# Optimization experiments

Hardware: AMD Instinct MI355X
Metric: run time of the kernel (lower is better)

The kernel has to match this reference:

```python
import jax, jax.numpy as jnp
import numpy as np

H = 256        # hidden_size
MAX_LEN = 200  # position table has MAX_LEN+1 rows
B = 4096       # number of sessions


def setup_inputs() -> dict:
    rng = np.random.RandomState(0)
    # ragged session lengths in [10, 100)
    seq_len = rng.randint(10, 100, size=B).astype(np.int64)
    T = int(seq_len.sum())
    # reverse positions: len-1, ..., 1, 0 per session (as the torch code uses)
    reverse_pos = np.concatenate([np.arange(l - 1, -1, -1) for l in seq_len]).astype(np.int64)

    key = jax.random.key(0)
    ks = jax.random.split(key, 8)
    def lin(k, fin, fout):
        # torch Linear init ~ U(-1/sqrt(fin), 1/sqrt(fin)); store as [fin, fout]
        lim = 1.0 / np.sqrt(fin)
        kw, kb = jax.random.split(k)
        W = jax.random.uniform(kw, (fin, fout), jnp.float32, -lim, lim)
        b = jax.random.uniform(kb, (fout,), jnp.float32, -lim, lim)
        return W, b

    hidden = jax.random.normal(ks[0], (T, H), jnp.float32)
    pos_table = jax.random.normal(ks[1], (MAX_LEN + 1, H), jnp.float32)
    W_pos, b_pos = lin(ks[2], 2 * H, H)   # W_pos_inter
    W1, b1 = lin(ks[3], H, H)             # W_1_inter
    W2, b2 = lin(ks[4], H, H)             # W_2_inter
    qw, qb = lin(ks[5], H, 1)             # q_inter

    return {
        "hidden": hidden,
        "pos_table": pos_table,
        "W_pos": W_pos, "b_pos": b_pos,
        "W1": W1, "b1": b1,
        "W2": W2, "b2": b2,
        "qw": qw, "qb": qb,
        "seq_len": jnp.asarray(seq_len),
        "reverse_pos": jnp.asarray(reverse_pos),
    }


def reference(hidden, pos_table, W_pos, b_pos, W1, b1, W2, b2, qw, qb, seq_len, reverse_pos):
    T = hidden.shape[0]
    nb = seq_len.shape[0]
    # segment id per token (sessions are contiguous)
    seg = jnp.repeat(jnp.arange(nb), seq_len, total_repeat_length=T)  # [T]
    # per-session mean, gathered back per token (v_mean_repeat_concat)
    sess_mean = jax.ops.segment_sum(hidden, seg, num_segments=nb)
    sess_mean = sess_mean / seq_len[:, None].astype(hidden.dtype)
    v_mean = sess_mean[seg]                                           # [T, H]
    # position-augmented hidden: tanh(W_pos_inter([hidden; pos_emb]))
    pos_emb = pos_table[reverse_pos]                                  # [T, H]
    pos_hidden = jnp.tanh(jnp.concatenate([hidden, pos_emb], -1) @ W_pos + b_pos)
    # alpha = q_inter(sigmoid(W_1_inter(v_mean) + W_2_inter(pos_hidden)))
    gate = jax.nn.sigmoid(v_mean @ W1 + b1 + pos_hidden @ W2 + b2)
    alpha = gate @ qw + qb                                            # [T, 1]
    # per-session weighted sum of hidden
    h_s = jax.ops.segment_sum(alpha * hidden, seg, num_segments=nb)   # [B, H]
    return h_s
```

## Files before the change

kernel.cpp:

```cpp
#include <hip/hip_runtime.h>
#include <hip/hip_bf16.h>
#include <stdint.h>

#define HD 256
#define BM 128
#define APAD 8
#define ASTRIDE (HD + APAD)

typedef __bf16 bf16x8 __attribute__((ext_vector_type(8)));
typedef float f32x4 __attribute__((ext_vector_type(4)));
typedef unsigned short ushort8v __attribute__((ext_vector_type(8)));
typedef unsigned short us4 __attribute__((ext_vector_type(4)));

__device__ __forceinline__ unsigned short f2bf(float f) {
    unsigned int x = __float_as_uint(f);
    unsigned int r = (x + 0x7FFFu + ((x >> 16) & 1u)) >> 16;
    return (unsigned short)r;
}

__global__ void scan_kernel(const int* __restrict__ seq_len, int* __restrict__ offsets, int B) {
    __shared__ int sums[256];
    int tid = threadIdx.x;
    int per = (B + 255) / 256;
    int b0 = tid * per;
    int local[32];
    int tot = 0;
    for (int i = 0; i < per && i < 32; ++i) {
        int b = b0 + i;
        int v = (b < B) ? seq_len[b] : 0;
        local[i] = tot;
        tot += v;
    }
    sums[tid] = tot;
    __syncthreads();
    for (int off = 1; off < 256; off <<= 1) {
        int v = (tid >= off) ? sums[tid - off] : 0;
        __syncthreads();
        sums[tid] += v;
        __syncthreads();
    }
    int start = sums[tid] - tot;
    for (int i = 0; i < per && i < 32; ++i) {
        int b = b0 + i;
        if (b < B) offsets[b] = start + local[i];
    }
    if (tid == 255) offsets[B] = sums[255];
}

__global__ void mean_kernel(const float* __restrict__ hidden, const int* __restrict__ offsets,
                            unsigned short* __restrict__ mean_bf, unsigned short* __restrict__ hb,
                            int* __restrict__ seg) {
    int b = blockIdx.x;
    int s = offsets[b], e = offsets[b + 1];
    int tid = threadIdx.x;
    for (int t = s + tid; t < e; t += 256) seg[t] = b;
    int g = tid >> 6, c = tid & 63;
    float4 acc = {0.f, 0.f, 0.f, 0.f};
    for (int t = s + g; t < e; t += 4) {
        const float4 v = *reinterpret_cast<const float4*>(hidden + (size_t)t * HD + c * 4);
        acc.x += v.x; acc.y += v.y; acc.z += v.z; acc.w += v.w;
        if (hb) {
            us4 pk;
            pk[0] = f2bf(v.x); pk[1] = f2bf(v.y); pk[2] = f2bf(v.z); pk[3] = f2bf(v.w);
            *reinterpret_cast<us4*>(hb + (size_t)t * HD + c * 4) = pk;
        }
    }
    __shared__ float4 part[4][64];
    part[g][c] = acc;
    __syncthreads();
    if (g == 0) {
        float4 a0 = part[0][c], a1 = part[1][c], a2 = part[2][c], a3 = part[3][c];
        float inv = 1.0f / (float)(e - s);
        us4 pk;
        pk[0] = f2bf((a0.x + a1.x + a2.x + a3.x) * inv);
        pk[1] = f2bf((a0.y + a1.y + a2.y + a3.y) * inv);
        pk[2] = f2bf((a0.z + a1.z + a2.z + a3.z) * inv);
        pk[3] = f2bf((a0.w + a1.w + a2.w + a3.w) * inv);
        *reinterpret_cast<us4*>(mean_bf + (size_t)b * HD + c * 4) = pk;
    }
}

__global__ void transpose_kernel(const float* __restrict__ Wp, const float* __restrict__ W1,
                                 const float* __restrict__ W2,
                                 unsigned short* __restrict__ WphT, unsigned short* __restrict__ WpbT,
                                 unsigned short* __restrict__ W1T, unsigned short* __restrict__ W2T) {
    int n = blockIdx.x;
    int k = threadIdx.x;
    WphT[n * HD + k] = f2bf(Wp[k * HD + n]);
    WpbT[n * HD + k] = f2bf(Wp[(HD + k) * HD + n]);
    W1T[n * HD + k]  = f2bf(W1[k * HD + n]);
    W2T[n * HD + k]  = f2bf(W2[k * HD + n]);
}

__global__ __launch_bounds__(256) void small_gemm_kernel(
    const unsigned short* __restrict__ mean_bf, int Mu, int nbu,
    const float* __restrict__ pos_table, int Mp,
    const unsigned short* __restrict__ W1T, const unsigned short* __restrict__ WpbT,
    const float* __restrict__ b1, const float* __restrict__ b2, const float* __restrict__ bp,
    float* __restrict__ u, float* __restrict__ P2) {
    __shared__ __align__(16) unsigned short As[16][ASTRIDE];
    int tid = threadIdx.x;
    bool isU = (int)blockIdx.x < nbu;
    int m0 = isU ? blockIdx.x * 16 : (blockIdx.x - nbu) * 16;
    int M  = isU ? Mu : Mp;
    const unsigned short* BT = isU ? W1T : WpbT;
    float* out = isU ? u : P2;

    {
        int row = tid >> 4;
        int colg = (tid & 15) * 16;
        int m = m0 + row;
        if (isU) {
            ushort8v v0 = {0,0,0,0,0,0,0,0}, v1 = {0,0,0,0,0,0,0,0};
            if (m < M) {
                v0 = *reinterpret_cast<const ushort8v*>(mean_bf + (size_t)m * HD + colg);
                v1 = *reinterpret_cast<const ushort8v*>(mean_bf + (size_t)m * HD + colg + 8);
            }
            *reinterpret_cast<ushort8v*>(&As[row][colg])     = v0;
            *reinterpret_cast<ushort8v*>(&As[row][colg + 8]) = v1;
        } else {
            float4 f[4] = {{0,0,0,0},{0,0,0,0},{0,0,0,0},{0,0,0,0}};
            if (m < M) {
                const float4* p = reinterpret_cast<const float4*>(pos_table + (size_t)m * HD + colg);
                f[0] = p[0]; f[1] = p[1]; f[2] = p[2]; f[3] = p[3];
            }
            ushort8v v0, v1;
            v0[0]=f2bf(f[0].x); v0[1]=f2bf(f[0].y); v0[2]=f2bf(f[0].z); v0[3]=f2bf(f[0].w);
            v0[4]=f2bf(f[1].x); v0[5]=f2bf(f[1].y); v0[6]=f2bf(f[1].z); v0[7]=f2bf(f[1].w);
            v1[0]=f2bf(f[2].x); v1[1]=f2bf(f[2].y); v1[2]=f2bf(f[2].z); v1[3]=f2bf(f[2].w);
            v1[4]=f2bf(f[3].x); v1[5]=f2bf(f[3].y); v1[6]=f2bf(f[3].z); v1[7]=f2bf(f[3].w);
            *reinterpret_cast<ushort8v*>(&As[row][colg])     = v0;
            *reinterpret_cast<ushort8v*>(&As[row][colg + 8]) = v1;
        }
    }
    __syncthreads();

    int wave = tid >> 6, lane = tid & 63, quad = lane >> 4, cc = lane & 15;
    int nb = wave * 64;
    f32x4 acc4[4];
    for (int i = 0; i < 4; ++i) acc4[i] = (f32x4){0.f, 0.f, 0.f, 0.f};

    bf16x8 wfp[4];
    for (int nf = 0; nf < 4; ++nf)
        wfp[nf] = *reinterpret_cast<const bf16x8*>(BT + (size_t)(nb + nf * 16 + cc) * HD + quad * 8);
    for (int kc8 = 0; kc8 < 8; ++kc8) {
        int kc = kc8 * 32;
        bf16x8 wfc[4];
        for (int nf = 0; nf < 4; ++nf) wfc[nf] = wfp[nf];
        if (kc8 < 7)
            for (int nf = 0; nf < 4; ++nf)
                wfp[nf] = *reinterpret_cast<const bf16x8*>(BT + (size_t)(nb + nf * 16 + cc) * HD + kc + 32 + quad * 8);
        bf16x8 af = *reinterpret_cast<const bf16x8*>(&As[cc][kc + quad * 8]);
        for (int nf = 0; nf < 4; ++nf)
            acc4[nf] = __builtin_amdgcn_mfma_f32_16x16x32_bf16(af, wfc[nf], acc4[nf], 0, 0, 0);
    }
    for (int nf = 0; nf < 4; ++nf)
        for (int r = 0; r < 4; ++r) {
            int row = m0 + quad * 4 + r;
            int col = nb + nf * 16 + cc;
            if (row < M) {
                float bias = isU ? (b1[col] + b2[col]) : bp[col];
                out[(size_t)row * HD + col] = acc4[nf][r] + bias;
            }
        }
}

__global__ __launch_bounds__(256, 2) void main_kernel(
    const float* __restrict__ hidden, const unsigned short* __restrict__ hb, int T,
    const unsigned short* __restrict__ WphT,
    const unsigned short* __restrict__ W2T,
    const float* __restrict__ P2,
    const float* __restrict__ u,
    const float* __restrict__ qw, const float* __restrict__ qb,
    const int* __restrict__ rp, const int* __restrict__ seg,
    float* __restrict__ alpha) {
    __shared__ __align__(16) unsigned short Ah[BM][ASTRIDE];
    __shared__ int rp_s[BM];
    __shared__ int seg_s[BM];
    __shared__ float alpha_s[BM];

    int tid = threadIdx.x;
    int t0 = blockIdx.x * BM;
    int wave = tid >> 6, lane = tid & 63, quad = lane >> 4, cc = lane & 15;
    int mb = wave * 64;

    bf16x8 afp[4];
    #pragma unroll
    for (int mf = 0; mf < 4; ++mf)
        afp[mf] = *reinterpret_cast<const bf16x8*>(WphT + (size_t)(mb + mf * 16 + cc) * HD + quad * 8);

    {
        int rbase = tid >> 2;
        #pragma unroll
        for (int half = 0; half < 2; ++half) {
            int row = rbase + half * 64;
            int t = t0 + row;
            if (hb) {
                #pragma unroll
                for (int i = 0; i < 8; ++i) {
                    int cg = (tid & 3) * 8 + 32 * i;
                    ushort8v v = {0,0,0,0,0,0,0,0};
                    if (t < T) v = *reinterpret_cast<const ushort8v*>(hb + (size_t)t * HD + cg);
                    *reinterpret_cast<ushort8v*>(&Ah[row][cg]) = v;
                }
            } else {
                #pragma unroll
                for (int i = 0; i < 8; ++i) {
                    int cg = (tid & 3) * 8 + 32 * i;
                    float4 f0 = {0,0,0,0}, f1 = {0,0,0,0};
                    if (t < T) {
                        const float4* p = reinterpret_cast<const float4*>(hidden + (size_t)t * HD + cg);
                        f0 = p[0]; f1 = p[1];
                    }
                    ushort8v pk;
                    pk[0] = f2bf(f0.x); pk[1] = f2bf(f0.y); pk[2] = f2bf(f0.z); pk[3] = f2bf(f0.w);
                    pk[4] = f2bf(f1.x); pk[5] = f2bf(f1.y); pk[6] = f2bf(f1.z); pk[7] = f2bf(f1.w);
                    *reinterpret_cast<ushort8v*>(&Ah[row][cg]) = pk;
                }
            }
        }
    }
    if (tid < BM) {
        int t = t0 + tid;
        rp_s[tid]  = (t < T) ? rp[t] : 0;
        seg_s[tid] = (t < T) ? seg[t] : 0;
        alpha_s[tid] = qb[0];
    }
    __syncthreads();

    f32x4 acc[32];
    #pragma unroll
    for (int i = 0; i < 32; ++i) acc[i] = (f32x4){0.f, 0.f, 0.f, 0.f};

    for (int kc8 = 0; kc8 < 8; ++kc8) {
        int kc = kc8 * 32;
        bf16x8 afc[4];
        #pragma unroll
        for (int mf = 0; mf < 4; ++mf) afc[mf] = afp[mf];
        if (kc8 < 7)
            #pragma unroll
            for (int mf = 0; mf < 4; ++mf)
                afp[mf] = *reinterpret_cast<const bf16x8*>(WphT + (size_t)(mb + mf * 16 + cc) * HD + kc + 32 + quad * 8);
        #pragma unroll
        for (int nf = 0; nf < 8; ++nf) {
            bf16x8 bfr = *reinterpret_cast<const bf16x8*>(&Ah[nf * 16 + cc][kc + quad * 8]);
            #pragma unroll
            for (int mf = 0; mf < 4; ++mf)
                acc[mf * 8 + nf] = __builtin_amdgcn_mfma_f32_16x16x32_bf16(afc[mf], bfr, acc[mf * 8 + nf], 0, 0, 0);
        }
    }
    __syncthreads();

    bf16x8 wfp[4];
    #pragma unroll
    for (int nf = 0; nf < 4; ++nf)
        wfp[nf] = *reinterpret_cast<const bf16x8*>(W2T + (size_t)(mb + nf * 16 + cc) * HD + quad * 8);

    #pragma unroll
    for (int mf = 0; mf < 4; ++mf)
        #pragma unroll
        for (int nf = 0; nf < 8; ++nf) {
            int token = nf * 16 + cc;
            int h0 = mb + mf * 16 + quad * 4;
            const float4 p2v = *reinterpret_cast<const float4*>(P2 + (size_t)rp_s[token] * HD + h0);
            us4 pk;
            {
                float v0 = acc[mf * 8 + nf][0] + p2v.x;
                float v1 = acc[mf * 8 + nf][1] + p2v.y;
                float v2 = acc[mf * 8 + nf][2] + p2v.z;
                float v3 = acc[mf * 8 + nf][3] + p2v.w;
                float e0 = __expf(2.f * v0), e1 = __expf(2.f * v1);
                float e2 = __expf(2.f * v2), e3 = __expf(2.f * v3);
                pk[0] = f2bf(1.f - 2.f / (e0 + 1.f));
                pk[1] = f2bf(1.f - 2.f / (e1 + 1.f));
                pk[2] = f2bf(1.f - 2.f / (e2 + 1.f));
                pk[3] = f2bf(1.f - 2.f / (e3 + 1.f));
            }
            *reinterpret_cast<us4*>(&Ah[token][h0]) = pk;
            acc[mf * 8 + nf] = (f32x4){0.f, 0.f, 0.f, 0.f};
        }
    __syncthreads();

    for (int kc8 = 0; kc8 < 8; ++kc8) {
        int kc = kc8 * 32;
        bf16x8 wfc[4];
        #pragma unroll
        for (int nf = 0; nf < 4; ++nf) wfc[nf] = wfp[nf];
        if (kc8 < 7)
            #pragma unroll
            for (int nf = 0; nf < 4; ++nf)
                wfp[nf] = *reinterpret_cast<const bf16x8*>(W2T + (size_t)(mb + nf * 16 + cc) * HD + kc + 32 + quad * 8);
        #pragma unroll
        for (int mf = 0; mf < 8; ++mf) {
            bf16x8 af = *reinterpret_cast<const bf16x8*>(&Ah[mf * 16 + cc][kc + quad * 8]);
            #pragma unroll
            for (int nf = 0; nf < 4; ++nf)
                acc[mf * 4 + nf] = __builtin_amdgcn_mfma_f32_16x16x32_bf16(af, wfc[nf], acc[mf * 4 + nf], 0, 0, 0);
        }
    }

    float qwv[4];
    #pragma unroll
    for (int nf = 0; nf < 4; ++nf) qwv[nf] = qw[mb + nf * 16 + cc];
    #pragma unroll
    for (int mf = 0; mf < 8; ++mf)
        #pragma unroll
        for (int r = 0; r < 4; ++r) {
            int token = mf * 16 + quad * 4 + r;
            const float* urow = u + (size_t)seg_s[token] * HD;
            float s = 0.f;
            #pragma unroll
            for (int nf = 0; nf < 4; ++nf) {
                float g = acc[mf * 4 + nf][r] + urow[mb + nf * 16 + cc];
                g = 1.0f / (1.0f + __expf(-g));
                s += g * qwv[nf];
            }
            s += __shfl_xor(s, 1);
            s += __shfl_xor(s, 2);
            s += __shfl_xor(s, 4);
            s += __shfl_xor(s, 8);
            if (cc == 0) atomicAdd(&alpha_s[token], s);
        }
    __syncthreads();
    if (tid < BM) {
        int t = t0 + tid;
        if (t < T) alpha[t] = alpha_s[tid];
    }
}

__global__ void hs_kernel(const float* __restrict__ hidden, const unsigned short* __restrict__ hb,
                          const float* __restrict__ alpha,
                          const int* __restrict__ offsets, float* __restrict__ out) {
    int b = blockIdx.x;
    int s = offsets[b], e = offsets[b + 1];
    int tid = threadIdx.x;
    __shared__ float al[256];
    for (int i = tid; i < e - s; i += 256) al[i] = alpha[s + i];
    __syncthreads();
    int g = tid >> 6, c = tid & 63;
    float4 acc = {0.f, 0.f, 0.f, 0.f};
    if (hb) {
        for (int t = s + g; t < e; t += 4) {
            float a = al[t - s];
            us4 v = *reinterpret_cast<const us4*>(hb + (size_t)t * HD + c * 4);
            acc.x += a * __uint_as_float(((unsigned)v[0]) << 16);
            acc.y += a * __uint_as_float(((unsigned)v[1]) << 16);
            acc.z += a * __uint_as_float(((unsigned)v[2]) << 16);
            acc.w += a * __uint_as_float(((unsigned)v[3]) << 16);
        }
    } else {
        for (int t = s + g; t < e; t += 4) {
            float a = al[t - s];
            const float4 v = *reinterpret_cast<const float4*>(hidden + (size_t)t * HD + c * 4);
            acc.x += a * v.x; acc.y += a * v.y; acc.z += a * v.z; acc.w += a * v.w;
        }
    }
    __shared__ float4 part[4][64];
    part[g][c] = acc;
    __syncthreads();
    if (g == 0) {
        float4 a0 = part[0][c], a1 = part[1][c], a2 = part[2][c], a3 = part[3][c];
        float4 m;
        m.x = a0.x + a1.x + a2.x + a3.x;
        m.y = a0.y + a1.y + a2.y + a3.y;
        m.z = a0.z + a1.z + a2.z + a3.z;
        m.w = a0.w + a1.w + a2.w + a3.w;
        *reinterpret_cast<float4*>(out + (size_t)b * HD + c * 4) = m;
    }
}

extern "C" void kernel_launch(void* const* d_in, const int* in_sizes, int n_in,
                              void* d_out, int out_size, void* d_ws, size_t ws_size,
                              hipStream_t stream) {
    (void)n_in; (void)out_size;
    const float* hidden    = (const float*)d_in[0];
    const float* pos_table = (const float*)d_in[1];
    const float* W_pos     = (const float*)d_in[2];
    const float* b_pos     = (const float*)d_in[3];
    const float* W1        = (const float*)d_in[4];
    const float* b1        = (const float*)d_in[5];
    const float* W2        = (const float*)d_in[6];
    const float* b2        = (const float*)d_in[7];
    const float* qw        = (const float*)d_in[8];
    const float* qb        = (const float*)d_in[9];
    const int* seq_len     = (const int*)d_in[10];
    const int* reverse_pos = (const int*)d_in[11];

    int T  = in_sizes[0] / HD;
    int B  = in_sizes[10];
    int NP = in_sizes[1] / HD;

    char* ws = (char*)d_ws;
    char* ws_end = ws + ws_size;
    auto carve = [&](size_t bytes) -> char* {
        char* p = ws;
        ws += (bytes + 255) & ~(size_t)255;
        return p;
    };
    int* offsets          = (int*)carve((size_t)(B + 1) * sizeof(int));
    int* seg              = (int*)carve((size_t)T * sizeof(int));
    unsigned short* meanb = (unsigned short*)carve((size_t)B * HD * 2);
    float* u              = (float*)carve((size_t)B * HD * sizeof(float));
    float* P2             = (float*)carve((size_t)NP * HD * sizeof(float));
    unsigned short* WphT  = (unsigned short*)carve((size_t)HD * HD * 2);
    unsigned short* WpbT  = (unsigned short*)carve((size_t)HD * HD * 2);
    unsigned short* W1T   = (unsigned short*)carve((size_t)HD * HD * 2);
    unsigned short* W2T   = (unsigned short*)carve((size_t)HD * HD * 2);
    float* alpha          = (float*)carve((size_t)T * sizeof(float));
    unsigned short* hb    = nullptr;
    if ((size_t)(ws_end - ws) >= (size_t)T * HD * 2 + 256)
        hb = (unsigned short*)carve((size_t)T * HD * 2);

    int nbu = (B + 15) / 16;
    int nbp = (NP + 15) / 16;

    scan_kernel<<<1, 256, 0, stream>>>(seq_len, offsets, B);
    transpose_kernel<<<HD, HD, 0, stream>>>(W_pos, W1, W2, WphT, WpbT, W1T, W2T);
    mean_kernel<<<B, 256, 0, stream>>>(hidden, offsets, meanb, hb, seg);
    small_gemm_kernel<<<nbu + nbp, 256, 0, stream>>>(meanb, B, nbu, pos_table, NP,
                                                     W1T, WpbT, b1, b2, b_pos, u, P2);
    main_kernel<<<(T + BM - 1) / BM, 256, 0, stream>>>(hidden, hb, T, WphT, W2T, P2, u, qw, qb,
                                                       reverse_pos, seg, alpha);
    hs_kernel<<<B, 256, 0, stream>>>(hidden, hb, alpha, offsets, (float*)d_out);
}
```

Baseline: 585.0 us.

## Shrink main kernel token tile, use 8 waves per block, tile weight transpose

The main kernel's token tile drops from 128 to 64 tokens while block size doubles to 512 threads. Each of the 8 waves now owns 32 output features across the 64 tokens, so the accumulator footprint is much smaller. The second GEMM's operand roles are swapped so the alpha reduction runs across quads with two shuffles and vectorized u/qw loads. The weight transpose kernel now goes through a shared-memory 64x64 tile with coalesced reads and writes. The aim is higher occupancy and less register pressure, at the cost of reloading weight fragments for twice as many blocks.

```diff
diff --git a/kernel.cpp b/kernel.cpp
--- a/kernel.cpp
+++ b/kernel.cpp
@@ -3,7 +3,7 @@
 #include <stdint.h>
 
 #define HD 256
-#define BM 128
+#define BM 64
 #define APAD 8
 #define ASTRIDE (HD + APAD)
 
@@ -84,12 +84,50 @@
                                  const float* __restrict__ W2,
                                  unsigned short* __restrict__ WphT, unsigned short* __restrict__ WpbT,
                                  unsigned short* __restrict__ W1T, unsigned short* __restrict__ W2T) {
-    int n = blockIdx.x;
-    int k = threadIdx.x;
-    WphT[n * HD + k] = f2bf(Wp[k * HD + n]);
-    WpbT[n * HD + k] = f2bf(Wp[(HD + k) * HD + n]);
-    W1T[n * HD + k]  = f2bf(W1[k * HD + n]);
-    W2T[n * HD + k]  = f2bf(W2[k * HD + n]);
+    __shared__ unsigned short tile[64][72];
+    int bid = blockIdx.x;
+    int tid = threadIdx.x;
+    const float* src;
+    unsigned short* dst;
+    int k0, n0, kk;
+    if (bid < 32) {
+        int tk = bid >> 2, tn = bid & 3;
+        src = Wp; k0 = tk * 64; n0 = tn * 64;
+        if (k0 < 256) { dst = WphT; kk = k0; }
+        else          { dst = WpbT; kk = k0 - 256; }
+    } else if (bid < 48) {
+        int b2 = bid - 32;
+        src = W1; k0 = (b2 >> 2) * 64; n0 = (b2 & 3) * 64;
+        dst = W1T; kk = k0;
+    } else {
+        int b2 = bid - 48;
+        src = W2; k0 = (b2 >> 2) * 64; n0 = (b2 & 3) * 64;
+        dst = W2T; kk = k0;
+    }
+    {
+        int col = tid & 63;
+        int rbase = tid >> 6;
+        #pragma unroll
+        for (int i = 0; i < 16; ++i) {
+            int lrow = rbase + 4 * i;
+            tile[lrow][col] = f2bf(src[(size_t)(k0 + lrow) * HD + n0 + col]);
+        }
+    }
+    __syncthreads();
+    {
+        int nl = tid >> 2;
+        int kc0 = (tid & 3) * 16;
+        #pragma unroll
+        for (int j = 0; j < 4; ++j) {
+            int kc = kc0 + 4 * j;
+            us4 v;
+            v[0] = tile[kc + 0][nl];
+            v[1] = tile[kc + 1][nl];
+            v[2] = tile[kc + 2][nl];
+            v[3] = tile[kc + 3][nl];
+            *reinterpret_cast<us4*>(dst + (size_t)(n0 + nl) * HD + kk + kc) = v;
+        }
+    }
 }
 
 __global__ __launch_bounds__(256) void small_gemm_kernel(
@@ -165,7 +203,7 @@
         }
 }
 
-__global__ __launch_bounds__(256, 2) void main_kernel(
+__global__ __launch_bounds__(512, 4) void main_kernel(
     const float* __restrict__ hidden, const unsigned short* __restrict__ hb, int T,
     const unsigned short* __restrict__ WphT,
     const unsigned short* __restrict__ W2T,
@@ -182,41 +220,37 @@
     int tid = threadIdx.x;
     int t0 = blockIdx.x * BM;
     int wave = tid >> 6, lane = tid & 63, quad = lane >> 4, cc = lane & 15;
-    int mb = wave * 64;
-
-    bf16x8 afp[4];
-    #pragma unroll
-    for (int mf = 0; mf < 4; ++mf)
+    int mb = wave * 32;
+
+    bf16x8 afp[2];
+    #pragma unroll
+    for (int mf = 0; mf < 2; ++mf)
         afp[mf] = *reinterpret_cast<const bf16x8*>(WphT + (size_t)(mb + mf * 16 + cc) * HD + quad * 8);
 
     {
-        int rbase = tid >> 2;
-        #pragma unroll
-        for (int half = 0; half < 2; ++half) {
-            int row = rbase + half * 64;
-            int t = t0 + row;
-            if (hb) {
-                #pragma unroll
-                for (int i = 0; i < 8; ++i) {
-                    int cg = (tid & 3) * 8 + 32 * i;
-                    ushort8v v = {0,0,0,0,0,0,0,0};
-                    if (t < T) v = *reinterpret_cast<const ushort8v*>(hb + (size_t)t * HD + cg);
-                    *reinterpret_cast<ushort8v*>(&Ah[row][cg]) = v;
+        int row = tid >> 3;
+        int t = t0 + row;
+        if (hb) {
+            #pragma unroll
+            for (int i = 0; i < 4; ++i) {
+                int cg = (tid & 7) * 8 + 64 * i;
+                ushort8v v = {0,0,0,0,0,0,0,0};
+                if (t < T) v = *reinterpret_cast<const ushort8v*>(hb + (size_t)t * HD + cg);
+                *reinterpret_cast<ushort8v*>(&Ah[row][cg]) = v;
+            }
+        } else {
+            #pragma unroll
+            for (int i = 0; i < 4; ++i) {
+                int cg = (tid & 7) * 8 + 64 * i;
+                float4 f0 = {0,0,0,0}, f1 = {0,0,0,0};
+                if (t < T) {
+                    const float4* p = reinterpret_cast<const float4*>(hidden + (size_t)t * HD + cg);
+                    f0 = p[0]; f1 = p[1];
                 }
-            } else {
-                #pragma unroll
-                for (int i = 0; i < 8; ++i) {
-                    int cg = (tid & 3) * 8 + 32 * i;
-                    float4 f0 = {0,0,0,0}, f1 = {0,0,0,0};
-                    if (t < T) {
-                        const float4* p = reinterpret_cast<const float4*>(hidden + (size_t)t * HD + cg);
-                        f0 = p[0]; f1 = p[1];
-                    }
-                    ushort8v pk;
-                    pk[0] = f2bf(f0.x); pk[1] = f2bf(f0.y); pk[2] = f2bf(f0.z); pk[3] = f2bf(f0.w);
-                    pk[4] = f2bf(f1.x); pk[5] = f2bf(f1.y); pk[6] = f2bf(f1.z); pk[7] = f2bf(f1.w);
-                    *reinterpret_cast<ushort8v*>(&Ah[row][cg]) = pk;
-                }
+                ushort8v pk;
+                pk[0] = f2bf(f0.x); pk[1] = f2bf(f0.y); pk[2] = f2bf(f0.z); pk[3] = f2bf(f0.w);
+                pk[4] = f2bf(f1.x); pk[5] = f2bf(f1.y); pk[6] = f2bf(f1.z); pk[7] = f2bf(f1.w);
+                *reinterpret_cast<ushort8v*>(&Ah[row][cg]) = pk;
             }
         }
     }
@@ -228,47 +262,52 @@
     }
     __syncthreads();
 
-    f32x4 acc[32];
-    #pragma unroll
-    for (int i = 0; i < 32; ++i) acc[i] = (f32x4){0.f, 0.f, 0.f, 0.f};
+    f32x4 acc[2][4];
+    #pragma unroll
+    for (int i = 0; i < 2; ++i)
+        #pragma unroll
+        for (int j = 0; j < 4; ++j) acc[i][j] = (f32x4){0.f, 0.f, 0.f, 0.f};
 
     for (int kc8 = 0; kc8 < 8; ++kc8) {
         int kc = kc8 * 32;
-        bf16x8 afc[4];
-        #pragma unroll
-        for (int mf = 0; mf < 4; ++mf) afc[mf] = afp[mf];
+        bf16x8 afc[2];
+        #pragma unroll
+        for (int mf = 0; mf < 2; ++mf) afc[mf] = afp[mf];
         if (kc8 < 7)
             #pragma unroll
-            for (int mf = 0; mf < 4; ++mf)
+            for (int mf = 0; mf < 2; ++mf)
                 afp[mf] = *reinterpret_cast<const bf16x8*>(WphT + (size_t)(mb + mf * 16 + cc) * HD + kc + 32 + quad * 8);
-        #pragma unroll
-        for (int nf = 0; nf < 8; ++nf) {
-            bf16x8 bfr = *reinterpret_cast<const bf16x8*>(&Ah[nf * 16 + cc][kc + quad * 8]);
-            #pragma unroll
-            for (int mf = 0; mf < 4; ++mf)
-                acc[mf * 8 + nf] = __builtin_amdgcn_mfma_f32_16x16x32_bf16(afc[mf], bfr, acc[mf * 8 + nf], 0, 0, 0);
-        }
-    }
-    __syncthreads();
-
-    bf16x8 wfp[4];
-    #pragma unroll
-    for (int nf = 0; nf < 4; ++nf)
-        wfp[nf] = *reinterpret_cast<const bf16x8*>(W2T + (size_t)(mb + nf * 16 + cc) * HD + quad * 8);
-
-    #pragma unroll
-    for (int mf = 0; mf < 4; ++mf)
-        #pragma unroll
-        for (int nf = 0; nf < 8; ++nf) {
-            int token = nf * 16 + cc;
+        bf16x8 bfr[4];
+        #pragma unroll
+        for (int nf = 0; nf < 4; ++nf)
+            bfr[nf] = *reinterpret_cast<const bf16x8*>(&Ah[nf * 16 + cc][kc + quad * 8]);
+        #pragma unroll
+        for (int mf = 0; mf < 2; ++mf)
+            #pragma unroll
+            for (int nf = 0; nf < 4; ++nf)
+                acc[mf][nf] = __builtin_amdgcn_mfma_f32_16x16x32_bf16(afc[mf], bfr[nf], acc[mf][nf], 0, 0, 0);
+    }
+    __syncthreads();
+
+    bf16x8 wfp[2];
+    #pragma unroll
+    for (int mf = 0; mf < 2; ++mf)
+        wfp[mf] = *reinterpret_cast<const bf16x8*>(W2T + (size_t)(mb + mf * 16 + cc) * HD + quad * 8);
+
+    #pragma unroll
+    for (int nf = 0; nf < 4; ++nf) {
+        int token = nf * 16 + cc;
+        const float* p2row = P2 + (size_t)rp_s[token] * HD;
+        #pragma unroll
+        for (int mf = 0; mf < 2; ++mf) {
             int h0 = mb + mf * 16 + quad * 4;
-            const float4 p2v = *reinterpret_cast<const float4*>(P2 + (size_t)rp_s[token] * HD + h0);
+            const float4 p2v = *reinterpret_cast<const float4*>(p2row + h0);
             us4 pk;
             {
-                float v0 = acc[mf * 8 + nf][0] + p2v.x;
-                float v1 = acc[mf * 8 + nf][1] + p2v.y;
-                float v2 = acc[mf * 8 + nf][2] + p2v.z;
-                float v3 = acc[mf * 8 + nf][3] + p2v.w;
+                float v0 = acc[mf][nf][0] + p2v.x;
+                float v1 = acc[mf][nf][1] + p2v.y;
+                float v2 = acc[mf][nf][2] + p2v.z;
+                float v3 = acc[mf][nf][3] + p2v.w;
                 float e0 = __expf(2.f * v0), e1 = __expf(2.f * v1);
                 float e2 = __expf(2.f * v2), e3 = __expf(2.f * v3);
                 pk[0] = f2bf(1.f - 2.f / (e0 + 1.f));
@@ -277,50 +316,53 @@
                 pk[3] = f2bf(1.f - 2.f / (e3 + 1.f));
             }
             *reinterpret_cast<us4*>(&Ah[token][h0]) = pk;
-            acc[mf * 8 + nf] = (f32x4){0.f, 0.f, 0.f, 0.f};
-        }
+            acc[mf][nf] = (f32x4){0.f, 0.f, 0.f, 0.f};
+        }
+    }
     __syncthreads();
 
     for (int kc8 = 0; kc8 < 8; ++kc8) {
         int kc = kc8 * 32;
-        bf16x8 wfc[4];
-        #pragma unroll
-        for (int nf = 0; nf < 4; ++nf) wfc[nf] = wfp[nf];
+        bf16x8 wfc[2];
+        #pragma unroll
+        for (int mf = 0; mf < 2; ++mf) wfc[mf] = wfp[mf];
         if (kc8 < 7)
             #pragma unroll
-            for (int nf = 0; nf < 4; ++nf)
-                wfp[nf] = *reinterpret_cast<const bf16x8*>(W2T + (size_t)(mb + nf * 16 + cc) * HD + kc + 32 + quad * 8);
-        #pragma unroll
-        for (int mf = 0; mf < 8; ++mf) {
-            bf16x8 af = *reinterpret_cast<const bf16x8*>(&Ah[mf * 16 + cc][kc + quad * 8]);
-            #pragma unroll
-            for (int nf = 0; nf < 4; ++nf)
-                acc[mf * 4 + nf] = __builtin_amdgcn_mfma_f32_16x16x32_bf16(af, wfc[nf], acc[mf * 4 + nf], 0, 0, 0);
-        }
-    }
-
-    float qwv[4];
-    #pragma unroll
-    for (int nf = 0; nf < 4; ++nf) qwv[nf] = qw[mb + nf * 16 + cc];
-    #pragma unroll
-    for (int mf = 0; mf < 8; ++mf)
-        #pragma unroll
-        for (int r = 0; r < 4; ++r) {
-            int token = mf * 16 + quad * 4 + r;
-            const float* urow = u + (size_t)seg_s[token] * HD;
-            float s = 0.f;
-            #pragma unroll
-            for (int nf = 0; nf < 4; ++nf) {
-                float g = acc[mf * 4 + nf][r] + urow[mb + nf * 16 + cc];
+            for (int mf = 0; mf < 2; ++mf)
+                wfp[mf] = *reinterpret_cast<const bf16x8*>(W2T + (size_t)(mb + mf * 16 + cc) * HD + kc + 32 + quad * 8);
+        #pragma unroll
+        for (int nf = 0; nf < 4; ++nf) {
+            bf16x8 af = *reinterpret_cast<const bf16x8*>(&Ah[nf * 16 + cc][kc + quad * 8]);
+            #pragma unroll
+            for (int mf = 0; mf < 2; ++mf)
+                acc[mf][nf] = __builtin_amdgcn_mfma_f32_16x16x32_bf16(wfc[mf], af, acc[mf][nf], 0, 0, 0);
+        }
+    }
+
+    float4 qv[2];
+    #pragma unroll
+    for (int mf = 0; mf < 2; ++mf)
+        qv[mf] = *reinterpret_cast<const float4*>(qw + mb + mf * 16 + quad * 4);
+    #pragma unroll
+    for (int nf = 0; nf < 4; ++nf) {
+        int token = nf * 16 + cc;
+        const float* urow = u + (size_t)seg_s[token] * HD;
+        float s = 0.f;
+        #pragma unroll
+        for (int mf = 0; mf < 2; ++mf) {
+            int n0 = mb + mf * 16 + quad * 4;
+            const float4 uv = *reinterpret_cast<const float4*>(urow + n0);
+            #pragma unroll
+            for (int r = 0; r < 4; ++r) {
+                float g = acc[mf][nf][r] + ((const float*)&uv)[r];
                 g = 1.0f / (1.0f + __expf(-g));
-                s += g * qwv[nf];
-            }
-            s += __shfl_xor(s, 1);
-            s += __shfl_xor(s, 2);
-            s += __shfl_xor(s, 4);
-            s += __shfl_xor(s, 8);
-            if (cc == 0) atomicAdd(&alpha_s[token], s);
-        }
+                s += g * ((const float*)&qv[mf])[r];
+            }
+        }
+        s += __shfl_xor(s, 16);
+        s += __shfl_xor(s, 32);
+        if (quad == 0) atomicAdd(&alpha_s[token], s);
+    }
     __syncthreads();
     if (tid < BM) {
         int t = t0 + tid;
@@ -415,11 +457,11 @@
     int nbp = (NP + 15) / 16;
 
     scan_kernel<<<1, 256, 0, stream>>>(seq_len, offsets, B);
-    transpose_kernel<<<HD, HD, 0, stream>>>(W_pos, W1, W2, WphT, WpbT, W1T, W2T);
+    transpose_kernel<<<64, 256, 0, stream>>>(W_pos, W1, W2, WphT, WpbT, W1T, W2T);
     mean_kernel<<<B, 256, 0, stream>>>(hidden, offsets, meanb, hb, seg);
     small_gemm_kernel<<<nbu + nbp, 256, 0, stream>>>(meanb, B, nbu, pos_table, NP,
                                                      W1T, WpbT, b1, b2, b_pos, u, P2);
-    main_kernel<<<(T + BM - 1) / BM, 256, 0, stream>>>(hidden, hb, T, WphT, W2T, P2, u, qw, qb,
+    main_kernel<<<(T + BM - 1) / BM, 512, 0, stream>>>(hidden, hb, T, WphT, W2T, P2, u, qw, qb,
                                                        reverse_pos, seg, alpha);
     hs_kernel<<<B, 256, 0, stream>>>(hidden, hb, alpha, offsets, (float*)d_out);
 }
```

After: 561.1 us. 1.04x faster.
